# Optimization experiments

Hardware: AMD Instinct MI355X
Metric: run time of the kernel (lower is better)

## Reference

```python
import jax, jax.numpy as jnp
import numpy as np

B = 64        # batch_size (rejection-sampling proposals per column)
P = 200000    # p (number of spike-and-slab variables)
K = 10        # number of accepted samples kept per column
ZETA = 1.1
GAMMA = -0.1
BETA = 2.0 / 3.0
GZ_LOGRATIO = -GAMMA / ZETA


def setup_inputs() -> dict:
    key = jax.random.key(0)
    kZ, kU, ku = jax.random.split(key, 3)
    return {
        "Z": jax.random.normal(kZ, (B, P), dtype=jnp.float32),
        "U": jax.random.uniform(kU, (B, P), dtype=jnp.float32),
        "u": jax.random.uniform(ku, (K, P), dtype=jnp.float32),
        "gamma_alpha": jnp.ones((P,), dtype=jnp.float32),
        "logalpha": jnp.ones((P,), dtype=jnp.float32),
        "batch_size": B,
    }


def reference(Z, U, u, gamma_alpha, logalpha, batch_size):
    # --- MarsagliaTsampler ---
    alpha = jax.nn.relu(gamma_alpha) + 1.0          # [P]
    d = alpha - 1.0 / 3.0                            # [P]
    c = 1.0 / jnp.sqrt(9.0 * d)                      # [P]
    V = (1.0 + c * Z) ** 3                           # [B, P]
    cond1 = Z > -1.0 / c
    cond2 = jnp.log(U) < 0.5 * Z ** 2 + d - d * V + d * jnp.log(V)
    cond = cond1 & cond2                             # nan comparisons -> False, as in torch
    out = jnp.where(cond, d * V, 0.0)                # [B, P]
    # take the FIRST K accepted samples per column (stable compaction)
    order = jnp.where(cond, jnp.arange(batch_size)[:, None], batch_size)
    idx = jnp.argsort(order, axis=0)[:K]             # [K, P]
    theta = jnp.take_along_axis(out, idx, axis=0)    # [K, P]

    # --- hard-concrete spike-and-slab gate (training mode) ---
    z_mean = jax.nn.sigmoid(logalpha - BETA * GZ_LOGRATIO)          # [P]
    s = jax.nn.sigmoid((jnp.log(u) - jnp.log1p(-u) + logalpha) / BETA)  # [K, P]
    z = jnp.clip((ZETA - GAMMA) * s + GAMMA, 0.0, 1.0)              # [K, P]

    return z, z_mean, theta, alpha, logalpha
```

## Files before the change

kernel.cpp:

```cpp
#include <hip/hip_runtime.h>
#include <math.h>

#define KACC 10
#define NRG 4
#define RPG 3
#define SCOLS 64

__global__ __launch_bounds__(256)
void sss_kernel(const float* __restrict__ Z, const float* __restrict__ U,
                const float* __restrict__ uu, const float* __restrict__ ga,
                const float* __restrict__ la, float* __restrict__ out,
                int P, int B, int nbScan, int perK, int vec4)
{
#pragma clang fp contract(off)
    const size_t KP = (size_t)KACC * (size_t)P;
    float* o_z        = out;
    float* o_zmean    = out + KP;
    float* o_theta    = out + KP + (size_t)P;
    float* o_alpha    = out + 2 * KP + (size_t)P;
    float* o_logalpha = out + 2 * KP + 2 * (size_t)P;

    const int bid = blockIdx.x;

    if (bid < nbScan) {
        __shared__ float s_val[NRG * RPG][SCOLS];
        __shared__ int   s_msk[NRG][SCOLS];

        const int t    = threadIdx.x;
        const int lane = t & (SCOLS - 1);
        const int rg   = t >> 6;
        const int col  = bid * SCOLS + lane;
        const bool cok = (col < P);

        const float g = cok ? ga[col] : 1.0f;
        const float alpha = fmaxf(g, 0.0f) + 1.0f;
        const float d     = alpha - (1.0f / 3.0f);
        const float c     = 1.0f / sqrtf(9.0f * d);
        const float neg_inv_c = -(1.0f / c);

        {
            float zv[RPG], wv[RPG];
#pragma unroll
            for (int j = 0; j < RPG; ++j) {
                const int row = rg * RPG + j;
                const size_t off = (size_t)row * (size_t)P + (size_t)col;
                const bool ok = cok && (row < B);
                zv[j] = ok ? Z[off] : __int_as_float(0x7fc00000);
                wv[j] = ok ? U[off] : 1.0f;
            }
            int m = 0;
#pragma unroll
            for (int j = 0; j < RPG; ++j) {
                float z  = zv[j];
                float Uv = wv[j];
                float tt = 1.0f + c * z;
                float V  = (tt * tt) * tt;
                float rhs = ((0.5f * (z * z) + d) - d * V) + d * logf(V);
                bool acc = (z > neg_inv_c) && (logf(Uv) < rhs);
                m |= acc ? (1 << j) : 0;
                s_val[rg * RPG + j][lane] = d * V;
            }
            s_msk[rg][lane] = m;
        }
        __syncthreads();
        if (rg != 0) return;

        const int mask = s_msk[0][lane]
                       | (s_msk[1][lane] << RPG)
                       | (s_msk[2][lane] << (2 * RPG))
                       | (s_msk[3][lane] << (3 * RPG));

        float th[KACC];
#pragma unroll
        for (int k = 0; k < KACC; ++k) th[k] = 0.0f;
        int cnt = 0;
#pragma unroll
        for (int j = 0; j < NRG * RPG; ++j) {
            bool acc = ((mask >> j) & 1) && (cnt < KACC);
            float val = s_val[j][lane];
#pragma unroll
            for (int k = 0; k < KACC; ++k)
                th[k] = (acc && cnt == k) ? val : th[k];
            cnt += acc ? 1 : 0;
        }

        if (cnt < KACC) {
            for (int base = NRG * RPG; base < B; base += 4) {
                float zv[4], wv[4];
#pragma unroll
                for (int i = 0; i < 4; ++i) {
                    const int row = base + i;
                    const size_t off = (size_t)row * (size_t)P + (size_t)col;
                    const bool ok = cok && (row < B);
                    zv[i] = ok ? Z[off] : __int_as_float(0x7fc00000);
                    wv[i] = ok ? U[off] : 1.0f;
                }
#pragma unroll
                for (int i = 0; i < 4; ++i) {
                    float z  = zv[i];
                    float Uv = wv[i];
                    float tt = 1.0f + c * z;
                    float V  = (tt * tt) * tt;
                    float rhs = ((0.5f * (z * z) + d) - d * V) + d * logf(V);
                    bool acc = (z > neg_inv_c) && (logf(Uv) < rhs) && (cnt < KACC);
                    float val = d * V;
#pragma unroll
                    for (int k = 0; k < KACC; ++k)
                        th[k] = (acc && cnt == k) ? val : th[k];
                    cnt += acc ? 1 : 0;
                }
                if (cnt >= KACC) break;
            }
        }

        if (cok) {
#pragma unroll
            for (int k = 0; k < KACC; ++k)
                o_theta[(size_t)k * (size_t)P + (size_t)col] = th[k];
            o_alpha[col] = alpha;
        }

    } else {
        const int gb  = bid - nbScan;
        const int k   = gb / perK;
        const int blk = gb - k * perK;
        const float SHIFT = 0.060606062f;

        if (vec4) {
            const int P4 = P >> 2;
            const int i4 = blk * blockDim.x + threadIdx.x;
            if (i4 >= P4) return;

            const float4 u4  = reinterpret_cast<const float4*>(uu + (size_t)k * (size_t)P)[i4];
            const float4 la4 = reinterpret_cast<const float4*>(la)[i4];

            float4 z4;
            {
                const float* us = (const float*)&u4;
                const float* ls = (const float*)&la4;
                float* zs = (float*)&z4;
#pragma unroll
                for (int j = 0; j < 4; ++j) {
                    float x = ((__logf(us[j]) - __logf(1.0f - us[j])) + ls[j]) * 1.5f;
                    float s = 1.0f / (1.0f + __expf(-x));
                    float zz = 1.2f * s - 0.1f;
                    zs[j] = fminf(fmaxf(zz, 0.0f), 1.0f);
                }
            }
            reinterpret_cast<float4*>(o_z + (size_t)k * (size_t)P)[i4] = z4;

            if (k == 0) {
                const float* ls = (const float*)&la4;
                float4 zm4;
                float* zm = (float*)&zm4;
#pragma unroll
                for (int j = 0; j < 4; ++j)
                    zm[j] = 1.0f / (1.0f + __expf(-(ls[j] - SHIFT)));
                reinterpret_cast<float4*>(o_zmean)[i4]    = zm4;
                reinterpret_cast<float4*>(o_logalpha)[i4] = la4;
            }
        } else {
            const int p = blk * blockDim.x + threadIdx.x;
            if (p >= P) return;
            const float u = uu[(size_t)k * (size_t)P + (size_t)p];
            const float lalpha = la[p];
            float x = ((__logf(u) - __logf(1.0f - u)) + lalpha) * 1.5f;
            float s = 1.0f / (1.0f + __expf(-x));
            float zz = 1.2f * s - 0.1f;
            o_z[(size_t)k * (size_t)P + (size_t)p] = fminf(fmaxf(zz, 0.0f), 1.0f);
            if (k == 0) {
                o_zmean[p]    = 1.0f / (1.0f + __expf(-(lalpha - SHIFT)));
                o_logalpha[p] = lalpha;
            }
        }
    }
}

extern "C" void kernel_launch(void* const* d_in, const int* in_sizes, int n_in,
                              void* d_out, int out_size, void* d_ws, size_t ws_size,
                              hipStream_t stream) {
    const float* Z  = (const float*)d_in[0];
    const float* U  = (const float*)d_in[1];
    const float* uu = (const float*)d_in[2];
    const float* ga = (const float*)d_in[3];
    const float* la = (const float*)d_in[4];
    float* out = (float*)d_out;

    const int P = in_sizes[3];
    const int B = in_sizes[0] / P;
    const int K = in_sizes[2] / P;

    const int block  = 256;
    const int nbScan = (P + SCOLS - 1) / SCOLS;
    const int vec4   = (P % 4 == 0) ? 1 : 0;
    const int perK   = vec4 ? ((P / 4 + block - 1) / block)
                            : ((P + block - 1) / block);
    const int grid   = nbScan + K * perK;
    sss_kernel<<<grid, block, 0, stream>>>(Z, U, uu, ga, la, out, P, B, nbScan, perK, vec4);
}
```

Before: 16.51 us.

## Interleave scan and gate blocks; compact accepted samples via bit scan

Block indices now alternate between rejection-scan blocks and gate blocks, so both kinds of work are spread evenly across the GPU instead of all scan blocks being dispatched first. The first-stage compaction of accepted samples replaces the nested select loop with ffs/popc bit iteration over the acceptance mask. The aim is better load balance between heavier scan blocks and memory-bound gate blocks, plus fewer ALU ops in compaction. The ffs loop adds data-dependent LDS indexing.

```diff
diff --git a/kernel.cpp b/kernel.cpp
--- a/kernel.cpp
+++ b/kernel.cpp
@@ -10,7 +10,7 @@
 void sss_kernel(const float* __restrict__ Z, const float* __restrict__ U,
                 const float* __restrict__ uu, const float* __restrict__ ga,
                 const float* __restrict__ la, float* __restrict__ out,
-                int P, int B, int nbScan, int perK, int vec4)
+                int P, int B, int nbScan, int nbGate, int perK, int vec4)
 {
 #pragma clang fp contract(off)
     const size_t KP = (size_t)KACC * (size_t)P;
@@ -21,15 +21,22 @@
     float* o_logalpha = out + 2 * KP + 2 * (size_t)P;
 
     const int bid = blockIdx.x;
-
-    if (bid < nbScan) {
+    const int nPair = 2 * nbGate;
+    int sIdx = -1, gIdx = -1;
+    if (bid < nPair) {
+        if (bid & 1) gIdx = bid >> 1; else sIdx = bid >> 1;
+    } else {
+        sIdx = nbGate + (bid - nPair);
+    }
+
+    if (sIdx >= 0) {
         __shared__ float s_val[NRG * RPG][SCOLS];
         __shared__ int   s_msk[NRG][SCOLS];
 
         const int t    = threadIdx.x;
         const int lane = t & (SCOLS - 1);
         const int rg   = t >> 6;
-        const int col  = bid * SCOLS + lane;
+        const int col  = sIdx * SCOLS + lane;
         const bool cok = (col < P);
 
         const float g = cok ? ga[col] : 1.0f;
@@ -71,18 +78,19 @@
                        | (s_msk[3][lane] << (3 * RPG));
 
         float th[KACC];
-#pragma unroll
-        for (int k = 0; k < KACC; ++k) th[k] = 0.0f;
-        int cnt = 0;
-#pragma unroll
-        for (int j = 0; j < NRG * RPG; ++j) {
-            bool acc = ((mask >> j) & 1) && (cnt < KACC);
-            float val = s_val[j][lane];
-#pragma unroll
-            for (int k = 0; k < KACC; ++k)
-                th[k] = (acc && cnt == k) ? val : th[k];
-            cnt += acc ? 1 : 0;
-        }
+        int m = mask;
+#pragma unroll
+        for (int k = 0; k < KACC; ++k) {
+            float v = 0.0f;
+            if (m) {
+                const int idx = __ffs(m) - 1;
+                v = s_val[idx][lane];
+                m &= m - 1;
+            }
+            th[k] = v;
+        }
+        int cnt = __popc(mask);
+        cnt = (cnt > KACC) ? KACC : cnt;
 
         if (cnt < KACC) {
             for (int base = NRG * RPG; base < B; base += 4) {
@@ -121,9 +129,8 @@
         }
 
     } else {
-        const int gb  = bid - nbScan;
-        const int k   = gb / perK;
-        const int blk = gb - k * perK;
+        const int k   = gIdx / perK;
+        const int blk = gIdx - k * perK;
         const float SHIFT = 0.060606062f;
 
         if (vec4) {
@@ -195,6 +202,8 @@
     const int vec4   = (P % 4 == 0) ? 1 : 0;
     const int perK   = vec4 ? ((P / 4 + block - 1) / block)
                             : ((P + block - 1) / block);
-    const int grid   = nbScan + K * perK;
-    sss_kernel<<<grid, block, 0, stream>>>(Z, U, uu, ga, la, out, P, B, nbScan, perK, vec4);
+    const int nbGate = K * perK;
+    const int grid   = nbScan + nbGate;
+    sss_kernel<<<grid, block, 0, stream>>>(Z, U, uu, ga, la, out, P, B,
+                                           nbScan, nbGate, perK, vec4);
 }
```

Measured after the change: 18.47 us. 1.12x slower.

## Spread scan rows across 768-thread blocks and parallelize first-K selection with ballots

Applied to the files above, without the earlier changes.

Each scan block now has 12 wavefronts, one per proposal row, instead of 4 wavefronts handling 3 rows each. Acceptance bitmasks are gathered with wave ballots. The theta writes are split so that wavefront k finds the k-th accepted row and writes it, while another wavefront writes alpha. Only wavefront 0 falls back to the serial scan of the remaining rows, and only when some column has fewer than K acceptances, with a wave-wide exit test. The block size also grows to 768 for the elementwise gate path, which means fewer, larger blocks and possibly lower occupancy flexibility.

```diff
diff --git a/kernel.cpp b/kernel.cpp
--- a/kernel.cpp
+++ b/kernel.cpp
@@ -2,11 +2,10 @@
 #include <math.h>
 
 #define KACC 10
-#define NRG 4
-#define RPG 3
-#define SCOLS 64
+#define ROWS 12
+#define SC   64
 
-__global__ __launch_bounds__(256)
+__global__ __launch_bounds__(768)
 void sss_kernel(const float* __restrict__ Z, const float* __restrict__ U,
                 const float* __restrict__ uu, const float* __restrict__ ga,
                 const float* __restrict__ la, float* __restrict__ out,
@@ -23,101 +22,96 @@
     const int bid = blockIdx.x;
 
     if (bid < nbScan) {
-        __shared__ float s_val[NRG * RPG][SCOLS];
-        __shared__ int   s_msk[NRG][SCOLS];
+        __shared__ float s_val[ROWS][SC];
+        __shared__ unsigned long long s_rm[ROWS];
 
         const int t    = threadIdx.x;
-        const int lane = t & (SCOLS - 1);
-        const int rg   = t >> 6;
-        const int col  = bid * SCOLS + lane;
+        const int lane = t & 63;
+        const int grp  = t >> 6;
+        const int col  = bid * SC + lane;
         const bool cok = (col < P);
 
         const float g = cok ? ga[col] : 1.0f;
         const float alpha = fmaxf(g, 0.0f) + 1.0f;
         const float d     = alpha - (1.0f / 3.0f);
         const float c     = 1.0f / sqrtf(9.0f * d);
-        const float neg_inv_c = -(1.0f / c);
+        const float ni    = -(1.0f / c);
 
         {
-            float zv[RPG], wv[RPG];
-#pragma unroll
-            for (int j = 0; j < RPG; ++j) {
-                const int row = rg * RPG + j;
-                const size_t off = (size_t)row * (size_t)P + (size_t)col;
-                const bool ok = cok && (row < B);
-                zv[j] = ok ? Z[off] : __int_as_float(0x7fc00000);
-                wv[j] = ok ? U[off] : 1.0f;
-            }
-            int m = 0;
-#pragma unroll
-            for (int j = 0; j < RPG; ++j) {
-                float z  = zv[j];
-                float Uv = wv[j];
-                float tt = 1.0f + c * z;
-                float V  = (tt * tt) * tt;
-                float rhs = ((0.5f * (z * z) + d) - d * V) + d * logf(V);
-                bool acc = (z > neg_inv_c) && (logf(Uv) < rhs);
-                m |= acc ? (1 << j) : 0;
-                s_val[rg * RPG + j][lane] = d * V;
-            }
-            s_msk[rg][lane] = m;
+            const int row = grp;
+            const bool ok = cok && (row < B);
+            const size_t off = (size_t)row * (size_t)P + (size_t)col;
+            float z  = ok ? Z[off] : __int_as_float(0x7fc00000);
+            float Uv = ok ? U[off] : 1.0f;
+            float tt = 1.0f + c * z;
+            float V  = (tt * tt) * tt;
+            float rhs = ((0.5f * (z * z) + d) - d * V) + d * logf(V);
+            bool acc = (z > ni) && (logf(Uv) < rhs);
+            s_val[grp][lane] = d * V;
+            unsigned long long bm = __ballot(acc);
+            if (lane == 0) s_rm[grp] = bm;
         }
         __syncthreads();
-        if (rg != 0) return;
 
-        const int mask = s_msk[0][lane]
-                       | (s_msk[1][lane] << RPG)
-                       | (s_msk[2][lane] << (2 * RPG))
-                       | (s_msk[3][lane] << (3 * RPG));
+        int mask = 0;
+#pragma unroll
+        for (int r = 0; r < ROWS; ++r)
+            mask |= (int)((s_rm[r] >> lane) & 1ULL) << r;
+        const int pc = __popc(mask);
+
+        if (grp < KACC) {
+            if (cok && grp < pc) {
+                int m = mask;
+#pragma unroll
+                for (int s = 0; s < KACC - 1; ++s)
+                    if (s < grp) m &= m - 1;
+                const int idx = __ffs(m) - 1;
+                o_theta[(size_t)grp * (size_t)P + (size_t)col] = s_val[idx][lane];
+            }
+        } else if (grp == KACC) {
+            if (cok) o_alpha[col] = alpha;
+        }
+        if (grp != 0) return;
+
+        const bool incomplete = cok && (pc < KACC);
+        if (!__any(incomplete)) return;
 
         float th[KACC];
 #pragma unroll
         for (int k = 0; k < KACC; ++k) th[k] = 0.0f;
-        int cnt = 0;
+        int cnt = (pc > KACC) ? KACC : pc;
+
+        for (int base = ROWS; base < B; base += 4) {
+            float zv[4], wv[4];
 #pragma unroll
-        for (int j = 0; j < NRG * RPG; ++j) {
-            bool acc = ((mask >> j) & 1) && (cnt < KACC);
-            float val = s_val[j][lane];
+            for (int i = 0; i < 4; ++i) {
+                const int row = base + i;
+                const size_t off = (size_t)row * (size_t)P + (size_t)col;
+                const bool ok = cok && (row < B);
+                zv[i] = ok ? Z[off] : __int_as_float(0x7fc00000);
+                wv[i] = ok ? U[off] : 1.0f;
+            }
+#pragma unroll
+            for (int i = 0; i < 4; ++i) {
+                float z  = zv[i];
+                float Uv = wv[i];
+                float tt = 1.0f + c * z;
+                float V  = (tt * tt) * tt;
+                float rhs = ((0.5f * (z * z) + d) - d * V) + d * logf(V);
+                bool acc = (z > ni) && (logf(Uv) < rhs) && (cnt < KACC);
+                float val = d * V;
+#pragma unroll
+                for (int k = 0; k < KACC; ++k)
+                    th[k] = (acc && cnt == k) ? val : th[k];
+                cnt += acc ? 1 : 0;
+            }
+            if (__all(cnt >= KACC)) break;
+        }
+
+        if (incomplete) {
 #pragma unroll
             for (int k = 0; k < KACC; ++k)
-                th[k] = (acc && cnt == k) ? val : th[k];
-            cnt += acc ? 1 : 0;
-        }
-
-        if (cnt < KACC) {
-            for (int base = NRG * RPG; base < B; base += 4) {
-                float zv[4], wv[4];
-#pragma unroll
-                for (int i = 0; i < 4; ++i) {
-                    const int row = base + i;
-                    const size_t off = (size_t)row * (size_t)P + (size_t)col;
-                    const bool ok = cok && (row < B);
-                    zv[i] = ok ? Z[off] : __int_as_float(0x7fc00000);
-                    wv[i] = ok ? U[off] : 1.0f;
-                }
-#pragma unroll
-                for (int i = 0; i < 4; ++i) {
-                    float z  = zv[i];
-                    float Uv = wv[i];
-                    float tt = 1.0f + c * z;
-                    float V  = (tt * tt) * tt;
-                    float rhs = ((0.5f * (z * z) + d) - d * V) + d * logf(V);
-                    bool acc = (z > neg_inv_c) && (logf(Uv) < rhs) && (cnt < KACC);
-                    float val = d * V;
-#pragma unroll
-                    for (int k = 0; k < KACC; ++k)
-                        th[k] = (acc && cnt == k) ? val : th[k];
-                    cnt += acc ? 1 : 0;
-                }
-                if (cnt >= KACC) break;
-            }
-        }
-
-        if (cok) {
-#pragma unroll
-            for (int k = 0; k < KACC; ++k)
-                o_theta[(size_t)k * (size_t)P + (size_t)col] = th[k];
-            o_alpha[col] = alpha;
+                if (k >= pc) o_theta[(size_t)k * (size_t)P + (size_t)col] = th[k];
         }
 
     } else {
@@ -190,8 +184,8 @@
     const int B = in_sizes[0] / P;
     const int K = in_sizes[2] / P;
 
-    const int block  = 256;
-    const int nbScan = (P + SCOLS - 1) / SCOLS;
+    const int block  = 768;
+    const int nbScan = (P + SC - 1) / SC;
     const int vec4   = (P % 4 == 0) ? 1 : 0;
     const int perK   = vec4 ? ((P / 4 + block - 1) / block)
                             : ((P + block - 1) / block);
```

Result: slower. 25.25 us (+52.9%).
